# Kernel optimization log

Measured on AMD Instinct MI355X. Metric: run time of the kernel, lower is better.

The kernel has to match this reference:

```python
import jax, jax.numpy as jnp
import numpy as np

HEADS = 8


def setup_inputs() -> dict:
    key = jax.random.key(0)
    ks = jax.random.split(key, 12)
    B, H, W, C = 2, 128, 256, 256
    inner = C  # num_heads * dim_head = 8 * 32

    def p(k, shape):
        return jax.random.normal(k, shape, dtype=jnp.float32) * 0.02

    return {
        "x": jax.random.normal(ks[0], (B, H * W, C), dtype=jnp.float32),
        "Wq_h": p(ks[1], (C, inner)),
        "Wk_h": p(ks[2], (C, inner)),
        "Wv_h": p(ks[3], (C, inner)),
        "Wo_h": p(ks[4], (inner, C)),
        "bo_h": p(ks[5], (C,)),
        "Wq_w": p(ks[6], (C, inner)),
        "Wk_w": p(ks[7], (C, inner)),
        "Wv_w": p(ks[8], (C, inner)),
        "Wo_w": p(ks[9], (inner, C)),
        "bo_w": p(ks[10], (C,)),
        "h": H,
        "w": W,
    }


def reference(x, Wq_h, Wk_h, Wv_h, Wo_h, bo_h, Wq_w, Wk_w, Wv_w, Wo_w, bo_w, h, w):
    b, n, c = x.shape
    heads = HEADS
    d = Wq_h.shape[1] // heads  # dim_head
    scale = d ** -0.5
    xs = x.reshape(b, h, w, c)  # [B,H,W,C]

    def proj(Wm):
        # [B,H,W,heads,d]
        return (xs @ Wm).reshape(b, h, w, heads, d)

    # --- height-axis attention: each column attends across all rows ---
    q, k, v = proj(Wq_h), proj(Wk_h), proj(Wv_h)
    s = jnp.einsum('bxwnd,bywnd->bwnxy', q, k) * scale  # [B,W,heads,H,H]
    a = jax.nn.softmax(s, axis=-1)
    oh = jnp.einsum('bwnxy,bywnd->bxwnd', a, v).reshape(b, h, w, heads * d)
    oh = oh @ Wo_h + bo_h

    # --- width-axis attention: each row attends across all columns ---
    q, k, v = proj(Wq_w), proj(Wk_w), proj(Wv_w)
    s = jnp.einsum('bhxnd,bhynd->bhnxy', q, k) * scale  # [B,H,heads,W,W]
    a = jax.nn.softmax(s, axis=-1)
    ow = jnp.einsum('bhnxy,bhynd->bhxnd', a, v).reshape(b, h, w, heads * d)
    ow = ow @ Wo_w + bo_w

    return (oh + ow).reshape(b, n, c)
```

## Files before the change

kernel.cpp:

```cpp
#include <hip/hip_runtime.h>
#include <hip/hip_bf16.h>
#include <stdint.h>

typedef unsigned short u16;
typedef short bf16x8 __attribute__((ext_vector_type(8)));
typedef float f32x4  __attribute__((ext_vector_type(4)));
typedef float f32x16 __attribute__((ext_vector_type(16)));
typedef unsigned int u32x4 __attribute__((ext_vector_type(4)));

__device__ __forceinline__ u16 f2bf(float f) {
    uint32_t u = __builtin_bit_cast(uint32_t, f);
    u += 0x7fffu + ((u >> 16) & 1u);
    return (u16)(u >> 16);
}

#if __has_builtin(__builtin_amdgcn_exp2f)
#define EXP2(x) __builtin_amdgcn_exp2f(x)
#else
extern "C" __device__ float __ocml_native_exp2_f32(float);
#define EXP2(x) __ocml_native_exp2_f32(x)
#endif

#define MM 65536
#define CC 256

#define QSCALE (1.4426950408889634f * 0.17677669529663687f)

__device__ __forceinline__ int perm_h(int t) {
    return ((t >> 15) << 15) | ((t & 127) << 8) | ((t >> 7) & 255);
}

__global__ void prep_kernel(
    const float* __restrict__ Wq_h, const float* __restrict__ Wk_h, const float* __restrict__ Wv_h,
    const float* __restrict__ Wo_h, const float* __restrict__ bo_h,
    const float* __restrict__ Wq_w, const float* __restrict__ Wk_w, const float* __restrict__ Wv_w,
    const float* __restrict__ Wo_w, const float* __restrict__ bo_w,
    u16* __restrict__ Wh_t, u16* __restrict__ Ww_t,
    u16* __restrict__ Woh_t, u16* __restrict__ Wow_t,
    u16* __restrict__ Wocat, float* __restrict__ bias)
{
    const int tid = blockIdx.x * 256 + threadIdx.x;
    const int nth = gridDim.x * 256;

    for (int i = tid; i < 768 * 256; i += nth) {
        int n = i >> 8, kk = i & 255;
        int which = n >> 8, nn = n & 255;
        const float* Wsh = (which == 0) ? Wq_h : (which == 1) ? Wk_h : Wv_h;
        const float* Wsw = (which == 0) ? Wq_w : (which == 1) ? Wk_w : Wv_w;
        Wh_t[i] = f2bf(Wsh[kk * 256 + nn]);
        Ww_t[i] = f2bf(Wsw[kk * 256 + nn]);
    }
    for (int i = tid; i < 256 * 256; i += nth) {
        int n = i >> 8, k = i & 255;
        Woh_t[i] = f2bf(Wo_h[k * 256 + n]);
        Wow_t[i] = f2bf(Wo_w[k * 256 + n]);
    }
    for (int i = tid; i < 256 * 512; i += nth) {
        int n = i >> 9, k = i & 511;
        float v = (k < 256) ? Wo_h[k * 256 + n] : Wo_w[(k - 256) * 256 + n];
        Wocat[i] = f2bf(v);
    }
    for (int i = tid; i < 256; i += nth) bias[i] = bo_h[i] + bo_w[i];
}

__global__ __launch_bounds__(256) void xcvt_kernel(const float* __restrict__ x, u16* __restrict__ xb)
{
    int i = blockIdx.x * 256 + threadIdx.x;
    const int nth = gridDim.x * 256;
    const int total = MM * 256 / 8;
    for (; i < total; i += nth) {
        const float* ap = x + (size_t)i * 8;
        float4 f0 = *(const float4*)ap;
        float4 f1 = *(const float4*)(ap + 4);
        u16 o[8] = { f2bf(f0.x), f2bf(f0.y), f2bf(f0.z), f2bf(f0.w),
                     f2bf(f1.x), f2bf(f1.y), f2bf(f1.z), f2bf(f1.w) };
        *(int4*)(xb + (size_t)i * 8) = *(const int4*)o;
    }
}

template<int PH, int XB>
__global__ __launch_bounds__(256) void gemm_qk_kernel(
    const float* __restrict__ x, const u16* __restrict__ xb, const u16* __restrict__ Bt,
    u16* __restrict__ Qb, u16* __restrict__ Kb)
{
    constexpr int S = PH ? 128 : 256;
    constexpr int L = PH ? 7 : 8;
    const int K = 256;
    __shared__ u16 sh[128 * 128];
    u16* As = sh;
    u16* Bs = sh + 128 * 64;
    const int tid = threadIdx.x;
    const int lane = tid & 63, wave = tid >> 6;
    const int wm = wave & 1, wn = wave >> 1;
    const int l15 = lane & 15, lq = lane >> 4;

    const int id = blockIdx.x;
    const int xcd = id & 7, wq = id >> 3;
    const int mt = xcd * 64 + (wq >> 2), nt = wq & 3;
    const int m0 = mt * 128, n0 = nt * 128;

    f32x4 acc[4][4];
#pragma unroll
    for (int i = 0; i < 4; i++)
#pragma unroll
        for (int j = 0; j < 4; j++)
#pragma unroll
            for (int t = 0; t < 4; t++) acc[i][j][t] = 0.0f;

    for (int kt = 0; kt < K; kt += 64) {
        __syncthreads();
#pragma unroll
        for (int i = 0; i < 4; i++) {
            int cid = i * 256 + tid;
            int r = cid >> 3, sc = cid & 7;
            int gk = kt + ((sc ^ (r & 7)) << 3);
            int rm = PH ? perm_h(m0 + r) : (m0 + r);
            if constexpr (XB) {
                *(int4*)(As + (size_t)cid * 8) = *(const int4*)(xb + (size_t)rm * 256 + gk);
            } else {
                const float* ap = x + (size_t)rm * 256 + gk;
                float4 f0 = *(const float4*)ap;
                float4 f1 = *(const float4*)(ap + 4);
                u16 o[8] = { f2bf(f0.x), f2bf(f0.y), f2bf(f0.z), f2bf(f0.w),
                             f2bf(f1.x), f2bf(f1.y), f2bf(f1.z), f2bf(f1.w) };
                *(int4*)(As + (size_t)cid * 8) = *(const int4*)o;
            }
            *(int4*)(Bs + (size_t)cid * 8) = *(const int4*)(Bt + (size_t)(n0 + r) * K + gk);
        }
        __syncthreads();
#pragma unroll
        for (int ks = 0; ks < 2; ks++) {
            bf16x8 af[4], bfr[4];
#pragma unroll
            for (int i = 0; i < 4; i++) {
                int row = wm * 64 + i * 16 + l15;
                int ca  = ks * 4 + lq;
                af[i]  = *(const bf16x8*)(As + row * 64 + ((ca ^ (row & 7)) << 3));
                int nn  = wn * 64 + i * 16 + l15;
                bfr[i] = *(const bf16x8*)(Bs + nn * 64 + ((ca ^ (nn & 7)) << 3));
            }
#pragma unroll
            for (int i = 0; i < 4; i++)
#pragma unroll
                for (int j = 0; j < 4; j++)
                    acc[i][j] = __builtin_amdgcn_mfma_f32_16x16x32_bf16(af[i], bfr[j], acc[i][j], 0, 0, 0);
        }
    }

    const float scale = (nt < 2) ? (float)QSCALE : 1.0f;
    __syncthreads();
#pragma unroll
    for (int i = 0; i < 4; i++)
#pragma unroll
        for (int j = 0; j < 4; j++)
#pragma unroll
            for (int r = 0; r < 4; r++) {
                int row = wm * 64 + i * 16 + lq * 4 + r;
                int col = wn * 64 + j * 16 + l15;
                sh[row * 128 + (col ^ ((row & 7) << 3))] = f2bf(acc[i][j][r] * scale);
            }
    __syncthreads();

    u16* dstb = (nt < 2) ? Qb : Kb;
    const int head = (nt * 4 + wave) & 7;
    const int gi = m0 >> L;
    const int seqbase = m0 & (S - 1);
    u16* dst = dstb + ((size_t)(gi * 8 + head) * S + seqbase) * 32;
#pragma unroll
    for (int it = 0; it < 8; it++) {
        int row = it * 16 + (lane >> 2);
        int d0  = (lane & 3) * 8;
        int coll = wave * 32 + d0;
        int4 v = *(const int4*)(sh + row * 128 + (coll ^ ((row & 7) << 3)));
        *(int4*)(dst + (size_t)row * 32 + d0) = v;
    }
}

template<int PH, int XB>
__global__ __launch_bounds__(256) void gemm_vt_kernel(
    const u16* __restrict__ Wt, const float* __restrict__ x, const u16* __restrict__ xb,
    u16* __restrict__ Vb)
{
    constexpr int S = PH ? 128 : 256;
    const int K = 256;
    __shared__ u16 sh[128 * 128];
    u16* As = sh;
    u16* Bs = sh + 128 * 64;
    const int tid = threadIdx.x;
    const int lane = tid & 63, wave = tid >> 6;
    const int wm = wave & 1, wn = wave >> 1;
    const int l15 = lane & 15, lq = lane >> 4;
    const int m0 = blockIdx.y * 128, n0 = blockIdx.x * 128;

    f32x4 acc[4][4];
#pragma unroll
    for (int i = 0; i < 4; i++)
#pragma unroll
        for (int j = 0; j < 4; j++)
#pragma unroll
            for (int t = 0; t < 4; t++) acc[i][j][t] = 0.0f;

    for (int kt = 0; kt < K; kt += 64) {
        __syncthreads();
#pragma unroll
        for (int i = 0; i < 4; i++) {
            int cid = i * 256 + tid;
            int r = cid >> 3, sc = cid & 7;
            int gk = kt + ((sc ^ (r & 7)) << 3);
            *(int4*)(As + (size_t)cid * 8) = *(const int4*)(Wt + (size_t)(m0 + r) * K + gk);
            int cm = PH ? perm_h(n0 + r) : (n0 + r);
            if constexpr (XB) {
                *(int4*)(Bs + (size_t)cid * 8) = *(const int4*)(xb + (size_t)cm * 256 + gk);
            } else {
                const float* bp = x + (size_t)cm * 256 + gk;
                float4 f0 = *(const float4*)bp;
                float4 f1 = *(const float4*)(bp + 4);
                u16 o[8] = { f2bf(f0.x), f2bf(f0.y), f2bf(f0.z), f2bf(f0.w),
                             f2bf(f1.x), f2bf(f1.y), f2bf(f1.z), f2bf(f1.w) };
                *(int4*)(Bs + (size_t)cid * 8) = *(const int4*)o;
            }
        }
        __syncthreads();
#pragma unroll
        for (int ks = 0; ks < 2; ks++) {
            bf16x8 af[4], bfr[4];
#pragma unroll
            for (int i = 0; i < 4; i++) {
                int row = wm * 64 + i * 16 + l15;
                int ca  = ks * 4 + lq;
                af[i]  = *(const bf16x8*)(As + row * 64 + ((ca ^ (row & 7)) << 3));
                int nn  = wn * 64 + i * 16 + l15;
                bfr[i] = *(const bf16x8*)(Bs + nn * 64 + ((ca ^ (nn & 7)) << 3));
            }
#pragma unroll
            for (int i = 0; i < 4; i++)
#pragma unroll
                for (int j = 0; j < 4; j++)
                    acc[i][j] = __builtin_amdgcn_mfma_f32_16x16x32_bf16(af[i], bfr[j], acc[i][j], 0, 0, 0);
        }
    }

    __syncthreads();
#pragma unroll
    for (int i = 0; i < 4; i++)
#pragma unroll
        for (int j = 0; j < 4; j++)
#pragma unroll
            for (int r = 0; r < 4; r++) {
                int row = wm * 64 + i * 16 + lq * 4 + r;
                int col = wn * 64 + j * 16 + l15;
                sh[row * 128 + (col ^ ((row & 7) << 3))] = f2bf(acc[i][j][r]);
            }
    __syncthreads();

    const int gi = n0 >> (PH ? 7 : 8);
    const int seqbase = n0 & (S - 1);
#pragma unroll
    for (int it = 0; it < 8; it++) {
        int row = wave * 32 + it * 4 + (lane >> 4);
        int c0  = (lane & 15) * 8;
        int4 v = *(const int4*)(sh + row * 128 + (c0 ^ ((row & 7) << 3)));
        int ch = m0 + row;
        u16* dst = Vb + (((size_t)(gi * 8 + (ch >> 5)) * 32 + (ch & 31)) * S + seqbase);
        *(int4*)(dst + c0) = v;
    }
}

__global__ __launch_bounds__(256) void gemm_out_fused_kernel(
    const u16* __restrict__ Ah, const u16* __restrict__ Aw,
    const u16* __restrict__ Bcat, float* __restrict__ Cout, const float* __restrict__ bias)
{
    const int K = 512, N = 256;
    __shared__ u16 As[128 * 64];
    __shared__ u16 Bs[128 * 64];
    const int tid = threadIdx.x;
    const int lane = tid & 63, wave = tid >> 6;
    const int wm = wave & 1, wn = wave >> 1;
    const int l15 = lane & 15, lq = lane >> 4;

    const int id = blockIdx.x;
    const int xcd = id & 7, wq = id >> 3;
    const int mt = xcd * 64 + (wq >> 1), nt = wq & 1;
    const int m0 = mt * 128, n0 = nt * 128;

    f32x4 acc[4][4];
#pragma unroll
    for (int i = 0; i < 4; i++)
#pragma unroll
        for (int j = 0; j < 4; j++)
#pragma unroll
            for (int t = 0; t < 4; t++) acc[i][j][t] = 0.0f;

    for (int kt = 0; kt < K; kt += 64) {
        __syncthreads();
        const u16* Abase = (kt < 256) ? Ah : Aw;
        int koff = kt & 255;
#pragma unroll
        for (int i = 0; i < 4; i++) {
            int cid = i * 256 + tid;
            int r = cid >> 3, sc = cid & 7;
            int gs = (sc ^ (r & 7)) << 3;
            *(int4*)(As + (size_t)cid * 8) = *(const int4*)(Abase + (size_t)(m0 + r) * 256 + koff + gs);
            *(int4*)(Bs + (size_t)cid * 8) = *(const int4*)(Bcat + (size_t)(n0 + r) * K + kt + gs);
        }
        __syncthreads();
#pragma unroll
        for (int ks = 0; ks < 2; ks++) {
            bf16x8 af[4], bfr[4];
#pragma unroll
            for (int i = 0; i < 4; i++) {
                int row = wm * 64 + i * 16 + l15;
                int ca  = ks * 4 + lq;
                af[i]  = *(const bf16x8*)(As + row * 64 + ((ca ^ (row & 7)) << 3));
                int nn  = wn * 64 + i * 16 + l15;
                bfr[i] = *(const bf16x8*)(Bs + nn * 64 + ((ca ^ (nn & 7)) << 3));
            }
#pragma unroll
            for (int i = 0; i < 4; i++)
#pragma unroll
                for (int j = 0; j < 4; j++)
                    acc[i][j] = __builtin_amdgcn_mfma_f32_16x16x32_bf16(af[i], bfr[j], acc[i][j], 0, 0, 0);
        }
    }
#pragma unroll
    for (int i = 0; i < 4; i++)
#pragma unroll
        for (int j = 0; j < 4; j++)
#pragma unroll
            for (int r = 0; r < 4; r++) {
                int row = m0 + wm * 64 + i * 16 + lq * 4 + r;
                int col = n0 + wn * 64 + j * 16 + l15;
                Cout[(size_t)row * N + col] = acc[i][j][r] + bias[col];
            }
}

template<int MODE>
__global__ __launch_bounds__(256) void gemm_out_kernel(
    const u16* __restrict__ A16, const u16* __restrict__ Bt,
    float* __restrict__ Cout, const float* __restrict__ bias)
{
    const int K = 256, N = 256;
    __shared__ u16 As[128 * 64];
    __shared__ u16 Bs[128 * 64];
    const int tid = threadIdx.x;
    const int lane = tid & 63, wave = tid >> 6;
    const int wm = wave & 1, wn = wave >> 1;
    const int l15 = lane & 15, lq = lane >> 4;
    const int m0 = blockIdx.y * 128, n0 = blockIdx.x * 128;

    f32x4 acc[4][4];
#pragma unroll
    for (int i = 0; i < 4; i++)
#pragma unroll
        for (int j = 0; j < 4; j++)
#pragma unroll
            for (int t = 0; t < 4; t++) acc[i][j][t] = 0.0f;

    for (int kt = 0; kt < K; kt += 64) {
        __syncthreads();
#pragma unroll
        for (int i = 0; i < 4; i++) {
            int cid = i * 256 + tid;
            int r = cid >> 3, sc = cid & 7;
            int gk = kt + ((sc ^ (r & 7)) << 3);
            *(int4*)(As + (size_t)cid * 8) = *(const int4*)(A16 + (size_t)(m0 + r) * K + gk);
            *(int4*)(Bs + (size_t)cid * 8) = *(const int4*)(Bt + (size_t)(n0 + r) * K + gk);
        }
        __syncthreads();
#pragma unroll
        for (int ks = 0; ks < 2; ks++) {
            bf16x8 af[4], bfr[4];
#pragma unroll
            for (int i = 0; i < 4; i++) {
                int row = wm * 64 + i * 16 + l15;
                int ca  = ks * 4 + lq;
                af[i]  = *(const bf16x8*)(As + row * 64 + ((ca ^ (row & 7)) << 3));
                int nn  = wn * 64 + i * 16 + l15;
                bfr[i] = *(const bf16x8*)(Bs + nn * 64 + ((ca ^ (nn & 7)) << 3));
            }
#pragma unroll
            for (int i = 0; i < 4; i++)
#pragma unroll
                for (int j = 0; j < 4; j++)
                    acc[i][j] = __builtin_amdgcn_mfma_f32_16x16x32_bf16(af[i], bfr[j], acc[i][j], 0, 0, 0);
        }
    }
#pragma unroll
    for (int i = 0; i < 4; i++)
#pragma unroll
        for (int j = 0; j < 4; j++)
#pragma unroll
            for (int r = 0; r < 4; r++) {
                int row = m0 + wm * 64 + i * 16 + lq * 4 + r;
                int col = n0 + wn * 64 + j * 16 + l15;
                size_t idx = (size_t)row * N + col;
                if (MODE == 1) Cout[idx] = acc[i][j][r] + bias[col];
                else           Cout[idx] += acc[i][j][r];
            }
}

template<int S, int PH, int NT>
__global__ __launch_bounds__(NT) void attn_kernel(
    const u16* __restrict__ Qb, const u16* __restrict__ Kb,
    const u16* __restrict__ Vb, u16* __restrict__ att)
{
    constexpr int NC = S / 32;
    const int tid = threadIdx.x;
    const int lane = tid & 63;
    const int wave = tid >> 6;
    const int ln = lane & 31;
    const int lh = lane >> 5;

    const int bid = blockIdx.x;
    const int head = bid & 7;
    const int gi = bid >> 3;
    const int qs = wave * 32;
    const int g = gi * 8 + head;

    const u16* Qg = Qb + (size_t)g * S * 32;
    const u16* Kg = Kb + (size_t)g * S * 32;
    const u16* Vg = Vb + (size_t)g * 32 * S;

    const u16* qp = Qg + (qs + ln) * 32 + lh * 8;
    bf16x8 bq0 = *(const bf16x8*)qp;
    bf16x8 bq1 = *(const bf16x8*)(qp + 16);

    f32x16 kz;
#pragma unroll
    for (int t = 0; t < 16; t++) kz[t] = 0.0f;
    asm("" : "+v"(kz));

    float rs[4] = {0.0f, 0.0f, 0.0f, 0.0f};
    f32x16 oacc;
#pragma unroll
    for (int t = 0; t < 16; t++) oacc[t] = 0.0f;

    const u16* kp0 = Kg + ln * 32 + lh * 8;
    const u16* vp0 = Vg + ln * S + lh * 8;
    bf16x8 ak0 = *(const bf16x8*)kp0;
    bf16x8 ak1 = *(const bf16x8*)(kp0 + 16);
    bf16x8 bv0 = *(const bf16x8*)vp0;
    bf16x8 bv1 = *(const bf16x8*)(vp0 + 16);

    for (int c = 0; c < NC; c++) {
        f32x16 z = __builtin_amdgcn_mfma_f32_32x32x16_bf16(ak0, bq0, kz, 0, 0, 0);
        z = __builtin_amdgcn_mfma_f32_32x32x16_bf16(ak1, bq1, z, 0, 0, 0);

        int cn = (c + 1 < NC) ? c + 1 : c;
        const u16* kp = kp0 + cn * 32 * 32;
        const u16* vp = vp0 + cn * 32;
        bf16x8 nk0 = *(const bf16x8*)kp;
        bf16x8 nk1 = *(const bf16x8*)(kp + 16);
        bf16x8 nv0 = *(const bf16x8*)vp;
        bf16x8 nv1 = *(const bf16x8*)(vp + 16);

        asm("" : "+v"(z));
        float p[16];
#pragma unroll
        for (int r = 0; r < 16; r++) { p[r] = EXP2(z[r]); rs[r & 3] += p[r]; }

        unsigned w[8];
#pragma unroll
        for (int t = 0; t < 8; t++) {
            unsigned d;
            asm("v_cvt_pk_bf16_f32 %0, %1, %2" : "=v"(d) : "v"(p[2 * t]), "v"(p[2 * t + 1]));
            w[t] = d;
        }
        auto s0 = __builtin_amdgcn_permlane32_swap(w[0], w[2], false, false);
        auto s1 = __builtin_amdgcn_permlane32_swap(w[1], w[3], false, false);
        auto s2 = __builtin_amdgcn_permlane32_swap(w[4], w[6], false, false);
        auto s3 = __builtin_amdgcn_permlane32_swap(w[5], w[7], false, false);
        u32x4 a0 = { (unsigned)s0[0], (unsigned)s1[0], (unsigned)s0[1], (unsigned)s1[1] };
        u32x4 a1 = { (unsigned)s2[0], (unsigned)s3[0], (unsigned)s2[1], (unsigned)s3[1] };
        bf16x8 pa0 = __builtin_bit_cast(bf16x8, a0);
        bf16x8 pa1 = __builtin_bit_cast(bf16x8, a1);

        oacc = __builtin_amdgcn_mfma_f32_32x32x16_bf16(pa0, bv0, oacc, 0, 0, 0);
        oacc = __builtin_amdgcn_mfma_f32_32x32x16_bf16(pa1, bv1, oacc, 0, 0, 0);

        ak0 = nk0; ak1 = nk1; bv0 = nv0; bv1 = nv1;
    }

    float rsum = (rs[0] + rs[1]) + (rs[2] + rs[3]);
    rsum += __shfl_xor(rsum, 32);
    float inv = 1.0f / rsum;
#pragma unroll
    for (int r = 0; r < 16; r++) {
        int row = (r & 3) + ((r >> 2) << 3) + (lh << 2);
        float is = __shfl(inv, row);
        int seq = qs + row;
        int m = PH ? ((gi >> 8) * 32768 + seq * 256 + (gi & 255))
                   : (gi * 256 + seq);
        att[(size_t)m * 256 + head * 32 + ln] = f2bf(oacc[r] * is);
    }
}

extern "C" void kernel_launch(void* const* d_in, const int* in_sizes, int n_in,
                              void* d_out, int out_size, void* d_ws, size_t ws_size,
                              hipStream_t stream)
{
    (void)in_sizes; (void)n_in; (void)out_size;
    const float* x    = (const float*)d_in[0];
    const float* Wq_h = (const float*)d_in[1];
    const float* Wk_h = (const float*)d_in[2];
    const float* Wv_h = (const float*)d_in[3];
    const float* Wo_h = (const float*)d_in[4];
    const float* bo_h = (const float*)d_in[5];
    const float* Wq_w = (const float*)d_in[6];
    const float* Wk_w = (const float*)d_in[7];
    const float* Wv_w = (const float*)d_in[8];
    const float* Wo_w = (const float*)d_in[9];
    const float* bo_w = (const float*)d_in[10];

    const size_t NB = (size_t)MM * 256;
    u16* Qb   = (u16*)d_ws;
    u16* Kb   = Qb + NB;
    u16* Vb   = Kb + NB;
    u16* attb = Vb + NB;
    u16* xb   = attb + NB;
    const size_t WT = (size_t)2 * 768 * 256 + (size_t)2 * 256 * 256 + (size_t)256 * 512 + 512;
    const bool use_xb = ws_size >= (5 * NB + WT) * sizeof(u16);
    u16* wp = use_xb ? (xb + NB) : xb;
    u16* Wh_t  = wp;
    u16* Ww_t  = Wh_t + 768 * 256;
    u16* Woh_t = Ww_t + 768 * 256;
    u16* Wow_t = Woh_t + 256 * 256;
    u16* Wocat = Wow_t + 256 * 256;
    float* bias = (float*)(Wocat + 256 * 512);

    prep_kernel<<<512, 256, 0, stream>>>(Wq_h, Wk_h, Wv_h, Wo_h, bo_h,
                                         Wq_w, Wk_w, Wv_w, Wo_w, bo_w,
                                         Wh_t, Ww_t, Woh_t, Wow_t, Wocat, bias);
    if (use_xb)
        xcvt_kernel<<<8192, 256, 0, stream>>>(x, xb);

    if (use_xb) {
        gemm_qk_kernel<1, 1><<<2048, 256, 0, stream>>>(x, xb, Wh_t, Qb, Kb);
        gemm_vt_kernel<1, 1><<<dim3(512, 2), 256, 0, stream>>>(Wh_t + 512 * 256, x, xb, Vb);
        attn_kernel<128, 1, 256><<<4096, 256, 0, stream>>>(Qb, Kb, Vb, attb);

        gemm_qk_kernel<0, 1><<<2048, 256, 0, stream>>>(x, xb, Ww_t, Qb, Kb);
        gemm_vt_kernel<0, 1><<<dim3(512, 2), 256, 0, stream>>>(Ww_t + 512 * 256, x, xb, Vb);
        attn_kernel<256, 0, 512><<<2048, 512, 0, stream>>>(Qb, Kb, Vb, xb);

        gemm_out_fused_kernel<<<1024, 256, 0, stream>>>(attb, xb, Wocat,
                                                        (float*)d_out, bias);
    } else {
        gemm_qk_kernel<1, 0><<<2048, 256, 0, stream>>>(x, xb, Wh_t, Qb, Kb);
        gemm_vt_kernel<1, 0><<<dim3(512, 2), 256, 0, stream>>>(Wh_t + 512 * 256, x, xb, Vb);
        attn_kernel<128, 1, 256><<<4096, 256, 0, stream>>>(Qb, Kb, Vb, attb);
        gemm_out_kernel<1><<<dim3(2, 512), 256, 0, stream>>>(attb, Woh_t, (float*)d_out, bias);

        gemm_qk_kernel<0, 0><<<2048, 256, 0, stream>>>(x, xb, Ww_t, Qb, Kb);
        gemm_vt_kernel<0, 0><<<dim3(512, 2), 256, 0, stream>>>(Ww_t + 512 * 256, x, xb, Vb);
        attn_kernel<256, 0, 512><<<2048, 512, 0, stream>>>(Qb, Kb, Vb, attb);
        gemm_out_kernel<2><<<dim3(2, 512), 256, 0, stream>>>(attb, Wow_t, (float*)d_out, nullptr);
    }
}
```

Measured before the change: 345.9 us.

## Store Q/K/V in MFMA fragment-native layout for contiguous attention loads

```diff
diff --git a/kernel.cpp b/kernel.cpp
--- a/kernel.cpp
+++ b/kernel.cpp
@@ -29,6 +29,7 @@
 __device__ __forceinline__ int perm_h(int t) {
     return ((t >> 15) << 15) | ((t & 127) << 8) | ((t >> 7) & 255);
 }
+
 
 __global__ void prep_kernel(
     const float* __restrict__ Wq_h, const float* __restrict__ Wk_h, const float* __restrict__ Wv_h,
@@ -166,14 +167,16 @@
     const int gi = m0 >> L;
     const int seqbase = m0 & (S - 1);
     u16* dst = dstb + ((size_t)(gi * 8 + head) * S + seqbase) * 32;
-#pragma unroll
-    for (int it = 0; it < 8; it++) {
-        int row = it * 16 + (lane >> 2);
-        int d0  = (lane & 3) * 8;
-        int coll = wave * 32 + d0;
-        int4 v = *(const int4*)(sh + row * 128 + (coll ^ ((row & 7) << 3)));
-        *(int4*)(dst + (size_t)row * 32 + d0) = v;
-    }
+    const int ln_ = lane & 31, lh_ = lane >> 5;
+#pragma unroll
+    for (int qt = 0; qt < 4; qt++)
+#pragma unroll
+        for (int half = 0; half < 2; half++) {
+            int row  = qt * 32 + ln_;
+            int colb = wave * 32 + half * 16 + lh_ * 8;
+            int4 v = *(const int4*)(sh + row * 128 + (colb ^ ((row & 7) << 3)));
+            *(int4*)(dst + qt * 1024 + half * 512 + lane * 8) = v;
+        }
 }
 
 template<int PH, int XB>
@@ -255,15 +258,18 @@
 
     const int gi = n0 >> (PH ? 7 : 8);
     const int seqbase = n0 & (S - 1);
-#pragma unroll
-    for (int it = 0; it < 8; it++) {
-        int row = wave * 32 + it * 4 + (lane >> 4);
-        int c0  = (lane & 15) * 8;
-        int4 v = *(const int4*)(sh + row * 128 + (c0 ^ ((row & 7) << 3)));
-        int ch = m0 + row;
-        u16* dst = Vb + (((size_t)(gi * 8 + (ch >> 5)) * 32 + (ch & 31)) * S + seqbase);
-        *(int4*)(dst + c0) = v;
-    }
+    const int head = (m0 >> 5) + wave;
+    u16* dst = Vb + ((size_t)(gi * 8 + head) * S + seqbase) * 32;
+    const int ln_ = lane & 31, lh_ = lane >> 5;
+#pragma unroll
+    for (int cl = 0; cl < 4; cl++)
+#pragma unroll
+        for (int half = 0; half < 2; half++) {
+            int row  = wave * 32 + ln_;
+            int colb = cl * 32 + half * 16 + lh_ * 8;
+            int4 v = *(const int4*)(sh + row * 128 + (colb ^ ((row & 7) << 3)));
+            *(int4*)(dst + cl * 1024 + half * 512 + lane * 8) = v;
+        }
 }
 
 __global__ __launch_bounds__(256) void gemm_out_fused_kernel(
@@ -419,11 +425,11 @@
 
     const u16* Qg = Qb + (size_t)g * S * 32;
     const u16* Kg = Kb + (size_t)g * S * 32;
-    const u16* Vg = Vb + (size_t)g * 32 * S;
-
-    const u16* qp = Qg + (qs + ln) * 32 + lh * 8;
+    const u16* Vg = Vb + (size_t)g * S * 32;
+
+    const u16* qp = Qg + (qs >> 5) * 1024 + lane * 8;
     bf16x8 bq0 = *(const bf16x8*)qp;
-    bf16x8 bq1 = *(const bf16x8*)(qp + 16);
+    bf16x8 bq1 = *(const bf16x8*)(qp + 512);
 
     f32x16 kz;
 #pragma unroll
@@ -435,24 +441,24 @@
 #pragma unroll
     for (int t = 0; t < 16; t++) oacc[t] = 0.0f;
 
-    const u16* kp0 = Kg + ln * 32 + lh * 8;
-    const u16* vp0 = Vg + ln * S + lh * 8;
+    const u16* kp0 = Kg + lane * 8;
+    const u16* vp0 = Vg + lane * 8;
     bf16x8 ak0 = *(const bf16x8*)kp0;
-    bf16x8 ak1 = *(const bf16x8*)(kp0 + 16);
+    bf16x8 ak1 = *(const bf16x8*)(kp0 + 512);
     bf16x8 bv0 = *(const bf16x8*)vp0;
-    bf16x8 bv1 = *(const bf16x8*)(vp0 + 16);
+    bf16x8 bv1 = *(const bf16x8*)(vp0 + 512);
 
     for (int c = 0; c < NC; c++) {
         f32x16 z = __builtin_amdgcn_mfma_f32_32x32x16_bf16(ak0, bq0, kz, 0, 0, 0);
         z = __builtin_amdgcn_mfma_f32_32x32x16_bf16(ak1, bq1, z, 0, 0, 0);
 
         int cn = (c + 1 < NC) ? c + 1 : c;
-        const u16* kp = kp0 + cn * 32 * 32;
-        const u16* vp = vp0 + cn * 32;
+        const u16* kp = kp0 + cn * 1024;
+        const u16* vp = vp0 + cn * 1024;
         bf16x8 nk0 = *(const bf16x8*)kp;
-        bf16x8 nk1 = *(const bf16x8*)(kp + 16);
+        bf16x8 nk1 = *(const bf16x8*)(kp + 512);
         bf16x8 nv0 = *(const bf16x8*)vp;
-        bf16x8 nv1 = *(const bf16x8*)(vp + 16);
+        bf16x8 nv1 = *(const bf16x8*)(vp + 512);
 
         asm("" : "+v"(z));
         float p[16];
```

Measured after the change: 322.8 us. 6.7% less time.
